# Kernel optimization log

Hardware: AMD Instinct MI355X
Metric: run time of the kernel (lower is better)

Reference implementation:

```python
import jax, jax.numpy as jnp
import numpy as np

K, T, F = 12000, 35, 7          # voxels, points-per-voxel (cfg.VOXEL_POINT_COUNT), point feature dim
B, D, H, W = 1, 10, 400, 352    # scatter grid: [batch, depth, cfg.INPUT_HEIGHT, cfg.INPUT_WIDTH]
C_OUT = 128
EPS = 1e-3                      # Keras BatchNormalization default epsilon


def setup_inputs() -> dict:
    key = jax.random.key(0)
    ks = jax.random.split(key, 20)
    # point features, with per-voxel padding (points beyond count are zero)
    feat = jax.random.normal(ks[0], (K, T, F), dtype=jnp.float32)
    counts = jax.random.randint(ks[1], (K,), 1, T + 1)
    valid = (jnp.arange(T)[None, :] < counts[:, None]).astype(jnp.float32)  # [K,T]
    feat = feat * valid[:, :, None]
    # voxel coordinates: (batch, d, h, w), in-range per dimension
    c0 = jax.random.randint(ks[2], (K,), 0, B)
    c1 = jax.random.randint(ks[3], (K,), 0, D)
    c2 = jax.random.randint(ks[4], (K,), 0, H)
    c3 = jax.random.randint(ks[5], (K,), 0, W)
    coordinate = jnp.stack([c0, c1, c2, c3], axis=1).astype(jnp.int32)  # [K,4]
    p = lambda i, shape: jax.random.normal(ks[i], shape, dtype=jnp.float32) * 0.1
    return {
        "input_feature": feat,
        "w1": p(6, (F, 16)), "b1": p(7, (16,)),
        "gamma1": 1.0 + p(8, (16,)), "beta1": p(9, (16,)),
        "mean1": p(10, (16,)), "var1": jax.random.uniform(ks[11], (16,), minval=0.5, maxval=1.5),
        "w2": p(12, (32, 64)), "b2": p(13, (64,)),
        "gamma2": 1.0 + p(14, (64,)), "beta2": p(15, (64,)),
        "mean2": p(16, (64,)), "var2": jax.random.uniform(ks[17], (64,), minval=0.5, maxval=1.5),
        "coordinate": coordinate,
        "batch_size": B,
    }


def vfe(x, mask, w, b, gamma, beta, mean, var):
    # Dense + relu (per point), inference BatchNorm, max-aggregate, tile-concat, mask
    dense = jax.nn.relu(jnp.einsum('ktf,fu->ktu', x, w) + b)
    pw = gamma * (dense - mean) * jax.lax.rsqrt(var + EPS) + beta  # [K,T,U]
    agg = jnp.max(pw, axis=1, keepdims=True)                       # [K,1,U]
    cat = jnp.concatenate([pw, jnp.broadcast_to(agg, pw.shape)], axis=2)  # [K,T,2U]
    return cat * mask


def reference(input_feature, w1, b1, gamma1, beta1, mean1, var1,
              w2, b2, gamma2, beta2, mean2, var2, coordinate, batch_size):
    # mask: point is valid if max over its features != 0
    mask = (jnp.max(input_feature, axis=2, keepdims=True) != 0).astype(input_feature.dtype)
    x = vfe(input_feature, mask, w1, b1, gamma1, beta1, mean1, var1)   # [K,T,32]
    x = vfe(x, mask, w2, b2, gamma2, beta2, mean2, var2)               # [K,T,128]
    voxelwise = jnp.max(x, axis=1)                                     # [K,128]
    out = jnp.zeros((batch_size, D, H, W, C_OUT), dtype=voxelwise.dtype)
    # tf.scatter_nd semantics: duplicate indices accumulate (add)
    out = out.at[coordinate[:, 0], coordinate[:, 1], coordinate[:, 2], coordinate[:, 3]].add(voxelwise)
    return out
```

## Files before the change

kernel.cpp:

```cpp
#include <hip/hip_runtime.h>

#define KVOX 12000
#define TPTS 35
#define FIN  7
#define DD   10
#define HH   400
#define WW   352
#define CO   128
#define EPSBN 1e-3f

__global__ __launch_bounds__(64) void vfe_scatter(
    const float* __restrict__ feat,
    const float* __restrict__ w1, const float* __restrict__ b1,
    const float* __restrict__ g1, const float* __restrict__ be1,
    const float* __restrict__ m1, const float* __restrict__ v1,
    const float* __restrict__ w2, const float* __restrict__ b2,
    const float* __restrict__ g2, const float* __restrict__ be2,
    const float* __restrict__ m2, const float* __restrict__ v2,
    const int* __restrict__ coord,
    float* __restrict__ out)
{
    const int k   = blockIdx.x;
    const int tid = threadIdx.x;

    __shared__ float sx[TPTS][FIN];
    __shared__ float smask[TPTS];
    __shared__ __align__(16) float sx2[TPTS][32];

    const float* fk = feat + (size_t)k * (TPTS * FIN);
    for (int i = tid; i < TPTS * FIN; i += 64)
        ((float*)sx)[i] = fk[i];
    __syncthreads();

    bool pred = false;
    if (tid < TPTS) {
        float mx = sx[tid][0];
        #pragma unroll
        for (int f = 1; f < FIN; ++f) mx = fmaxf(mx, sx[tid][f]);
        pred = (mx != 0.0f);
        smask[tid] = pred ? 1.0f : 0.0f;
    }
    unsigned long long bal = __ballot(pred);
    const int nvalid = __popcll(bal);
    __syncthreads();

    if (tid < 16) {
        const int u = tid;
        float w1c[FIN];
        #pragma unroll
        for (int f = 0; f < FIN; ++f) w1c[f] = w1[f * 16 + u];
        const float b     = b1[u];
        const float scale = g1[u] * rsqrtf(v1[u] + EPSBN);
        const float shift = be1[u] - m1[u] * scale;

        float agg = -INFINITY;
        float pw[TPTS];
        #pragma unroll
        for (int t = 0; t < TPTS; ++t) {
            float d = b;
            #pragma unroll
            for (int f = 0; f < FIN; ++f) d = fmaf(sx[t][f], w1c[f], d);
            d = fmaxf(d, 0.0f);
            float p = fmaf(d, scale, shift);
            agg = fmaxf(agg, p);
            pw[t] = p;
        }
        #pragma unroll
        for (int t = 0; t < TPTS; ++t) {
            const float mk = smask[t];
            sx2[t][u]      = pw[t] * mk;
            sx2[t][16 + u] = agg   * mk;
        }
    }
    __syncthreads();

    {
        const int v = tid;
        float w2c[32];
        #pragma unroll
        for (int u = 0; u < 32; ++u) w2c[u] = w2[u * 64 + v];
        const float b     = b2[v];
        const float scale = g2[v] * rsqrtf(v2[v] + EPSBN);
        const float shift = be2[v] - m2[v] * scale;

        float aggAll = -INFINITY;
        float voxA   = -INFINITY;
        #pragma unroll 5
        for (int t = 0; t < TPTS; ++t) {
            float d = b;
            const float4* xr = (const float4*)(&sx2[t][0]);
            #pragma unroll
            for (int q = 0; q < 8; ++q) {
                float4 xv = xr[q];
                d = fmaf(xv.x, w2c[4 * q + 0], d);
                d = fmaf(xv.y, w2c[4 * q + 1], d);
                d = fmaf(xv.z, w2c[4 * q + 2], d);
                d = fmaf(xv.w, w2c[4 * q + 3], d);
            }
            d = fmaxf(d, 0.0f);
            float p = fmaf(d, scale, shift);
            aggAll = fmaxf(aggAll, p);
            voxA   = fmaxf(voxA, p * smask[t]);
        }
        float voxB;
        if (nvalid == 0)          voxB = 0.0f;
        else if (nvalid < TPTS)   voxB = fmaxf(aggAll, 0.0f);
        else                      voxB = aggAll;

        const int4 c = ((const int4*)coord)[k];
        const int loc = (((c.x * DD + c.y) * HH + c.z) * WW + c.w);
        float* o = out + (size_t)loc * CO;
        atomicAdd(o + v,      voxA);
        atomicAdd(o + 64 + v, voxB);
    }
}

extern "C" void kernel_launch(void* const* d_in, const int* in_sizes, int n_in,
                              void* d_out, int out_size, void* d_ws, size_t ws_size,
                              hipStream_t stream) {
    const float* feat = (const float*)d_in[0];
    const float* w1   = (const float*)d_in[1];
    const float* b1   = (const float*)d_in[2];
    const float* g1   = (const float*)d_in[3];
    const float* be1  = (const float*)d_in[4];
    const float* m1   = (const float*)d_in[5];
    const float* v1   = (const float*)d_in[6];
    const float* w2   = (const float*)d_in[7];
    const float* b2   = (const float*)d_in[8];
    const float* g2   = (const float*)d_in[9];
    const float* be2  = (const float*)d_in[10];
    const float* m2   = (const float*)d_in[11];
    const float* v2   = (const float*)d_in[12];
    const int*   coord = (const int*)d_in[13];
    float* out = (float*)d_out;

    hipMemsetAsync(d_out, 0, (size_t)out_size * sizeof(float), stream);

    vfe_scatter<<<KVOX, 64, 0, stream>>>(feat, w1, b1, g1, be1, m1, v1,
                                         w2, b2, g2, be2, m2, v2, coord, out);
}
```

Before: 754.2 us.

## Replace atomic scatter with per-cell linked-list gather that writes output once

```diff
diff --git a/kernel.cpp b/kernel.cpp
--- a/kernel.cpp
+++ b/kernel.cpp
@@ -8,8 +8,140 @@
 #define WW   352
 #define CO   128
 #define EPSBN 1e-3f
-
-__global__ __launch_bounds__(64) void vfe_scatter(
+#define NCELL (DD * HH * WW)
+#define CELLS_PER_BLK 8
+
+__global__ __launch_bounds__(64) void vfe_compute(
+    const float* __restrict__ feat,
+    const float* __restrict__ w1, const float* __restrict__ b1,
+    const float* __restrict__ g1, const float* __restrict__ be1,
+    const float* __restrict__ m1, const float* __restrict__ v1,
+    const float* __restrict__ w2, const float* __restrict__ b2,
+    const float* __restrict__ g2, const float* __restrict__ be2,
+    const float* __restrict__ m2, const float* __restrict__ v2,
+    const int* __restrict__ coord,
+    float* __restrict__ vox,
+    int* __restrict__ head,
+    int* __restrict__ nxt)
+{
+    const int k   = blockIdx.x;
+    const int tid = threadIdx.x;
+
+    __shared__ float sx[TPTS][FIN];
+    __shared__ float smask[TPTS];
+    __shared__ __align__(16) float sx2[TPTS][32];
+
+    const float* fk = feat + (size_t)k * (TPTS * FIN);
+    for (int i = tid; i < TPTS * FIN; i += 64)
+        ((float*)sx)[i] = fk[i];
+    __syncthreads();
+
+    bool pred = false;
+    if (tid < TPTS) {
+        float mx = sx[tid][0];
+        #pragma unroll
+        for (int f = 1; f < FIN; ++f) mx = fmaxf(mx, sx[tid][f]);
+        pred = (mx != 0.0f);
+        smask[tid] = pred ? 1.0f : 0.0f;
+    }
+    unsigned long long bal = __ballot(pred);
+    const int nvalid = __popcll(bal);
+    __syncthreads();
+
+    if (tid < 16) {
+        const int u = tid;
+        float w1c[FIN];
+        #pragma unroll
+        for (int f = 0; f < FIN; ++f) w1c[f] = w1[f * 16 + u];
+        const float b     = b1[u];
+        const float scale = g1[u] * rsqrtf(v1[u] + EPSBN);
+        const float shift = be1[u] - m1[u] * scale;
+
+        float agg = -INFINITY;
+        float pw[TPTS];
+        #pragma unroll
+        for (int t = 0; t < TPTS; ++t) {
+            float d = b;
+            #pragma unroll
+            for (int f = 0; f < FIN; ++f) d = fmaf(sx[t][f], w1c[f], d);
+            d = fmaxf(d, 0.0f);
+            float p = fmaf(d, scale, shift);
+            agg = fmaxf(agg, p);
+            pw[t] = p;
+        }
+        #pragma unroll
+        for (int t = 0; t < TPTS; ++t) {
+            const float mk = smask[t];
+            sx2[t][u]      = pw[t] * mk;
+            sx2[t][16 + u] = agg   * mk;
+        }
+    }
+    __syncthreads();
+
+    {
+        const int v = tid;
+        float w2c[32];
+        #pragma unroll
+        for (int u = 0; u < 32; ++u) w2c[u] = w2[u * 64 + v];
+        const float b     = b2[v];
+        const float scale = g2[v] * rsqrtf(v2[v] + EPSBN);
+        const float shift = be2[v] - m2[v] * scale;
+
+        float aggAll = -INFINITY;
+        float voxA   = -INFINITY;
+        #pragma unroll 5
+        for (int t = 0; t < TPTS; ++t) {
+            float d = b;
+            const float4* xr = (const float4*)(&sx2[t][0]);
+            #pragma unroll
+            for (int q = 0; q < 8; ++q) {
+                float4 xv = xr[q];
+                d = fmaf(xv.x, w2c[4 * q + 0], d);
+                d = fmaf(xv.y, w2c[4 * q + 1], d);
+                d = fmaf(xv.z, w2c[4 * q + 2], d);
+                d = fmaf(xv.w, w2c[4 * q + 3], d);
+            }
+            d = fmaxf(d, 0.0f);
+            float p = fmaf(d, scale, shift);
+            aggAll = fmaxf(aggAll, p);
+            voxA   = fmaxf(voxA, p * smask[t]);
+        }
+        float voxB;
+        if (nvalid == 0)          voxB = 0.0f;
+        else if (nvalid < TPTS)   voxB = fmaxf(aggAll, 0.0f);
+        else                      voxB = aggAll;
+
+        float* vk = vox + (size_t)k * CO;
+        vk[v]      = voxA;
+        vk[64 + v] = voxB;
+
+        if (v == 0) {
+            const int4 c = ((const int4*)coord)[k];
+            const int loc = (((c.x * DD + c.y) * HH + c.z) * WW + c.w);
+            nxt[k] = atomicExch(&head[loc], k);
+        }
+    }
+}
+
+__global__ __launch_bounds__(256) void gather_out(
+    const float* __restrict__ vox, const int* __restrict__ head,
+    const int* __restrict__ nxt, float* __restrict__ out)
+{
+    const int tid  = threadIdx.x;
+    const int cell = blockIdx.x * CELLS_PER_BLK + (tid >> 5);
+    const int lane = tid & 31;
+
+    float4 acc = make_float4(0.f, 0.f, 0.f, 0.f);
+    int s = head[cell];
+    while (s >= 0) {
+        const float4 v = ((const float4*)vox)[s * 32 + lane];
+        acc.x += v.x; acc.y += v.y; acc.z += v.z; acc.w += v.w;
+        s = nxt[s];
+    }
+    ((float4*)out)[(size_t)cell * 32 + lane] = acc;
+}
+
+__global__ __launch_bounds__(64) void vfe_scatter_atomic(
     const float* __restrict__ feat,
     const float* __restrict__ w1, const float* __restrict__ b1,
     const float* __restrict__ g1, const float* __restrict__ be1,
@@ -22,16 +154,12 @@
 {
     const int k   = blockIdx.x;
     const int tid = threadIdx.x;
-
     __shared__ float sx[TPTS][FIN];
     __shared__ float smask[TPTS];
     __shared__ __align__(16) float sx2[TPTS][32];
-
     const float* fk = feat + (size_t)k * (TPTS * FIN);
-    for (int i = tid; i < TPTS * FIN; i += 64)
-        ((float*)sx)[i] = fk[i];
-    __syncthreads();
-
+    for (int i = tid; i < TPTS * FIN; i += 64) ((float*)sx)[i] = fk[i];
+    __syncthreads();
     bool pred = false;
     if (tid < TPTS) {
         float mx = sx[tid][0];
@@ -43,16 +171,14 @@
     unsigned long long bal = __ballot(pred);
     const int nvalid = __popcll(bal);
     __syncthreads();
-
     if (tid < 16) {
         const int u = tid;
         float w1c[FIN];
         #pragma unroll
         for (int f = 0; f < FIN; ++f) w1c[f] = w1[f * 16 + u];
-        const float b     = b1[u];
+        const float b = b1[u];
         const float scale = g1[u] * rsqrtf(v1[u] + EPSBN);
         const float shift = be1[u] - m1[u] * scale;
-
         float agg = -INFINITY;
         float pw[TPTS];
         #pragma unroll
@@ -68,23 +194,20 @@
         #pragma unroll
         for (int t = 0; t < TPTS; ++t) {
             const float mk = smask[t];
-            sx2[t][u]      = pw[t] * mk;
-            sx2[t][16 + u] = agg   * mk;
-        }
-    }
-    __syncthreads();
-
+            sx2[t][u] = pw[t] * mk;
+            sx2[t][16 + u] = agg * mk;
+        }
+    }
+    __syncthreads();
     {
         const int v = tid;
         float w2c[32];
         #pragma unroll
         for (int u = 0; u < 32; ++u) w2c[u] = w2[u * 64 + v];
-        const float b     = b2[v];
+        const float b = b2[v];
         const float scale = g2[v] * rsqrtf(v2[v] + EPSBN);
         const float shift = be2[v] - m2[v] * scale;
-
-        float aggAll = -INFINITY;
-        float voxA   = -INFINITY;
+        float aggAll = -INFINITY, voxA = -INFINITY;
         #pragma unroll 5
         for (int t = 0; t < TPTS; ++t) {
             float d = b;
@@ -100,17 +223,16 @@
             d = fmaxf(d, 0.0f);
             float p = fmaf(d, scale, shift);
             aggAll = fmaxf(aggAll, p);
-            voxA   = fmaxf(voxA, p * smask[t]);
+            voxA = fmaxf(voxA, p * smask[t]);
         }
         float voxB;
-        if (nvalid == 0)          voxB = 0.0f;
-        else if (nvalid < TPTS)   voxB = fmaxf(aggAll, 0.0f);
-        else                      voxB = aggAll;
-
+        if (nvalid == 0) voxB = 0.0f;
+        else if (nvalid < TPTS) voxB = fmaxf(aggAll, 0.0f);
+        else voxB = aggAll;
         const int4 c = ((const int4*)coord)[k];
         const int loc = (((c.x * DD + c.y) * HH + c.z) * WW + c.w);
         float* o = out + (size_t)loc * CO;
-        atomicAdd(o + v,      voxA);
+        atomicAdd(o + v, voxA);
         atomicAdd(o + 64 + v, voxB);
     }
 }
@@ -134,8 +256,24 @@
     const int*   coord = (const int*)d_in[13];
     float* out = (float*)d_out;
 
-    hipMemsetAsync(d_out, 0, (size_t)out_size * sizeof(float), stream);
-
-    vfe_scatter<<<KVOX, 64, 0, stream>>>(feat, w1, b1, g1, be1, m1, v1,
-                                         w2, b2, g2, be2, m2, v2, coord, out);
-}
+    const size_t voxB  = (size_t)KVOX * CO * sizeof(float);
+    const size_t headB = (size_t)NCELL * sizeof(int);
+    const size_t nxtB  = (size_t)KVOX * sizeof(int);
+    const size_t need  = voxB + headB + nxtB;
+
+    if (ws_size >= need) {
+        float* vox = (float*)d_ws;
+        int*   head = (int*)((char*)d_ws + voxB);
+        int*   nxt  = (int*)((char*)d_ws + voxB + headB);
+
+        hipMemsetAsync(head, 0xFF, headB, stream);
+        vfe_compute<<<KVOX, 64, 0, stream>>>(feat, w1, b1, g1, be1, m1, v1,
+                                             w2, b2, g2, be2, m2, v2, coord,
+                                             vox, head, nxt);
+        gather_out<<<NCELL / CELLS_PER_BLK, 256, 0, stream>>>(vox, head, nxt, out);
+    } else {
+        hipMemsetAsync(d_out, 0, (size_t)out_size * sizeof(float), stream);
+        vfe_scatter_atomic<<<KVOX, 64, 0, stream>>>(feat, w1, b1, g1, be1, m1, v1,
+                                                    w2, b2, g2, be2, m2, v2, coord, out);
+    }
+}
```

New measurement: 795.1 us. 5.4% more time.
